# Kernel tuning notes

Measured on AMD Instinct MI355X. Metric: run time of the kernel, lower is better.

Reference implementation:

```python
import jax, jax.numpy as jnp
import numpy as np

B, S, D, H, HS = 4, 2048, 1024, 16, 64
DFF = 4 * D
EPS = 1e-5


def setup_inputs() -> dict:
    key = jax.random.key(0)
    ks = jax.random.split(key, 16)
    std = 0.02
    return {
        "x": jax.random.normal(ks[0], (B, S, D), jnp.float32),
        "Wq": jax.random.normal(ks[1], (H, D, HS), jnp.float32) * std,
        "bq": jnp.zeros((H, HS), jnp.float32),
        "Wk": jax.random.normal(ks[2], (H, D, HS), jnp.float32) * std,
        "bk": jnp.zeros((H, HS), jnp.float32),
        "Wv": jax.random.normal(ks[3], (H, D, HS), jnp.float32) * std,
        "bv": jnp.zeros((H, HS), jnp.float32),
        "Wp": jax.random.normal(ks[4], (D, D), jnp.float32) * std,
        "bp": jnp.zeros((D,), jnp.float32),
        "ln1_w": jnp.ones((D,), jnp.float32),
        "ln1_b": jnp.zeros((D,), jnp.float32),
        "ln2_w": jnp.ones((D,), jnp.float32),
        "ln2_b": jnp.zeros((D,), jnp.float32),
        "W1": jax.random.normal(ks[5], (D, DFF), jnp.float32) * std,
        "b1": jnp.zeros((DFF,), jnp.float32),
        "W2": jax.random.normal(ks[6], (DFF, D), jnp.float32) * std,
        "b2": jnp.zeros((D,), jnp.float32),
    }


def _layernorm(x, w, b):
    mu = jnp.mean(x, axis=-1, keepdims=True)
    var = jnp.mean(jnp.square(x - mu), axis=-1, keepdims=True)
    return (x - mu) * jax.lax.rsqrt(var + EPS) * w + b


def _block(x, Wq, bq, Wk, bk, Wv, bv, Wp, bp, ln1_w, ln1_b, ln2_w, ln2_b, W1, b1, W2, b2):
    seq = x.shape[1]
    xn = _layernorm(x, ln1_w, ln1_b)
    # batched per-head projections: [B,H,S,HS]
    q = jnp.einsum('bsd,hdk->bhsk', xn, Wq) + bq[:, None, :]
    k = jnp.einsum('bsd,hdk->bhsk', xn, Wk) + bk[:, None, :]
    v = jnp.einsum('bsd,hdk->bhsk', xn, Wv) + bv[:, None, :]
    scores = jnp.einsum('bhsk,bhtk->bhst', q, k)
    mask = jnp.tril(jnp.ones((seq, seq), bool))
    # original: masked_fill(-inf) then divide by sqrt(head_size) -> equivalent
    scores = jnp.where(mask, scores / jnp.sqrt(jnp.float32(HS)), -jnp.inf)
    attn = jax.nn.softmax(scores, axis=-1)
    out = jnp.einsum('bhst,bhtk->bhsk', attn, v)
    out = out.transpose(0, 2, 1, 3).reshape(x.shape[0], seq, H * HS)
    att = out @ Wp + bp
    x = x + att
    xn2 = _layernorm(x, ln2_w, ln2_b)
    h = jax.nn.gelu(xn2 @ W1 + b1, approximate=False)  # torch nn.GELU default = exact
    ffn = h @ W2 + b2
    return x + ffn


def reference(x, Wq, bq, Wk, bk, Wv, bv, Wp, bp, ln1_w, ln1_b, ln2_w, ln2_b, W1, b1, W2, b2):
    out = _block(x, Wq, bq, Wk, bk, Wv, bv, Wp, bp, ln1_w, ln1_b, ln2_w, ln2_b, W1, b1, W2, b2)
    return out
```

## Files before the change

kernel.cpp:

```cpp
#include <hip/hip_runtime.h>
#include <hip/hip_bf16.h>

#define D_MODEL 1024
#define SEQ 2048
#define NH 16
#define HSZ 64
#define DFF_ 4096

typedef __attribute__((ext_vector_type(8))) short short8;
typedef __attribute__((ext_vector_type(4))) short short4v;
typedef __attribute__((ext_vector_type(4))) float f32x4;

static __device__ __forceinline__ short f2bf(float f) {
  unsigned u = __builtin_bit_cast(unsigned, f);
  u = u + 0x7fffu + ((u >> 16) & 1u);
  return (short)(u >> 16);
}

static __device__ __forceinline__ unsigned packbf2(float a, float b) {
  return (unsigned)(unsigned short)f2bf(a) | ((unsigned)(unsigned short)f2bf(b) << 16);
}

static __device__ __forceinline__ f32x4 mfma16(short8 a, short8 b, f32x4 c) {
  return __builtin_amdgcn_mfma_f32_16x16x32_bf16(a, b, c, 0, 0, 0);
}

static __device__ __forceinline__ void gld16(const short* g, short* l) {
  __builtin_amdgcn_global_load_lds((const __attribute__((address_space(1))) void*)g,
                                   (__attribute__((address_space(3))) void*)l, 16, 0, 0);
}

__global__ void transpose_qkv_kernel(const float* __restrict__ Wq, const float* __restrict__ Wk,
                                     const float* __restrict__ Wv, short* __restrict__ dst) {
  __shared__ float tile[32][33];
  const int z = blockIdx.z;
  const int which = z >> 4, hh = z & 15;
  const float* src = (which == 0 ? Wq : which == 1 ? Wk : Wv) + (long)hh * (D_MODEL * HSZ);
  const int c0 = blockIdx.x * 32, r0 = blockIdx.y * 32;
  const int tx = threadIdx.x, ty = threadIdx.y;
#pragma unroll
  for (int i = 0; i < 4; ++i)
    tile[ty + 8 * i][tx] = src[(long)(r0 + ty + 8 * i) * HSZ + c0 + tx];
  __syncthreads();
#pragma unroll
  for (int i = 0; i < 4; ++i)
    dst[((long)which * 1024 + hh * 64 + c0 + ty + 8 * i) * D_MODEL + r0 + tx] =
        f2bf(tile[tx][ty + 8 * i]);
}

__global__ void transpose_gen_kernel(const float* __restrict__ src, short* __restrict__ dst,
                                     int R, int C) {
  __shared__ float tile[32][33];
  const int c0 = blockIdx.x * 32, r0 = blockIdx.y * 32;
  const int tx = threadIdx.x, ty = threadIdx.y;
#pragma unroll
  for (int i = 0; i < 4; ++i)
    tile[ty + 8 * i][tx] = src[(long)(r0 + ty + 8 * i) * C + c0 + tx];
  __syncthreads();
#pragma unroll
  for (int i = 0; i < 4; ++i)
    dst[(long)(c0 + ty + 8 * i) * R + r0 + tx] = f2bf(tile[tx][ty + 8 * i]);
}

__global__ void v_transpose_kernel(const short* __restrict__ vb, short* __restrict__ vt) {
  __shared__ short tile[64 * 72];
  const int bh = blockIdx.y;
  const int t0 = blockIdx.x * 64;
  const long base = (long)bh * SEQ * HSZ;
  const int tid = threadIdx.x;
  const int r = tid >> 3, c = (tid & 7) * 8;
#pragma unroll
  for (int it = 0; it < 2; ++it) {
    const int rr = r + it * 32;
    *(short8*)&tile[rr * 72 + c] = *(const short8*)(vb + base + (long)(t0 + rr) * HSZ + c);
  }
  __syncthreads();
#pragma unroll
  for (int it = 0; it < 2; ++it) {
    const int rr = r + it * 32;
    short8 o;
#pragma unroll
    for (int u = 0; u < 8; ++u) o[u] = tile[(c + u) * 72 + rr];
    *(short8*)(vt + base + (long)rr * SEQ + t0 + c) = o;
  }
}

__global__ void ln_kernel(const float* __restrict__ x, const float* __restrict__ w,
                          const float* __restrict__ b, short* __restrict__ out) {
  const int row = blockIdx.x;
  const float* xr = x + (size_t)row * D_MODEL;
  const int t = threadIdx.x;
  float4 v = *(const float4*)(xr + t * 4);
  float s = v.x + v.y + v.z + v.w;
  float s2 = v.x * v.x + v.y * v.y + v.z * v.z + v.w * v.w;
#pragma unroll
  for (int o = 1; o < 64; o <<= 1) {
    s += __shfl_xor(s, o, 64);
    s2 += __shfl_xor(s2, o, 64);
  }
  __shared__ float ps[8];
  const int lane = t & 63, wid = t >> 6;
  if (lane == 0) { ps[wid] = s; ps[wid + 4] = s2; }
  __syncthreads();
  s = ps[0] + ps[1] + ps[2] + ps[3];
  s2 = ps[4] + ps[5] + ps[6] + ps[7];
  const float mu = s * (1.0f / D_MODEL);
  const float var = s2 * (1.0f / D_MODEL) - mu * mu;
  const float rs = rsqrtf(var + 1e-5f);
  float4 wv = *(const float4*)(w + t * 4);
  float4 bv = *(const float4*)(b + t * 4);
  short4v o4;
  o4[0] = f2bf((v.x - mu) * rs * wv.x + bv.x);
  o4[1] = f2bf((v.y - mu) * rs * wv.y + bv.y);
  o4[2] = f2bf((v.z - mu) * rs * wv.z + bv.z);
  o4[3] = f2bf((v.w - mu) * rs * wv.w + bv.w);
  *(short4v*)(out + (size_t)row * D_MODEL + t * 4) = o4;
}

#define BM 128
#define BN 128

template <int MODE>
__global__ void gemm_kernel(const short* __restrict__ A, const short* __restrict__ Bt,
                            const int K, const float* __restrict__ c0,
                            const float* __restrict__ c1, const float* __restrict__ c2,
                            const float* __restrict__ res, void* __restrict__ o0,
                            void* __restrict__ o1, void* __restrict__ o2) {
  __shared__ short As[2 * BM * 32];
  __shared__ short Bs[2 * BM * 32];
  const int tid = threadIdx.x;
  const int lane = tid & 63, wid = tid >> 6;
  const int wm = wid >> 1, wn = wid & 1;
  const int l16 = lane & 15, lg = lane >> 4;
  const long r0 = (long)blockIdx.y * BM;
  const long n0 = (long)blockIdx.x * BN;

  f32x4 acc[4][4];
#pragma unroll
  for (int m = 0; m < 4; ++m)
#pragma unroll
    for (int n = 0; n < 4; ++n) {
      f32x4 z = {0.f, 0.f, 0.f, 0.f};
      acc[m][n] = z;
    }

  const int sr = lane >> 2;
  const int sc = (lane & 3) * 8;
  const short* ga0 = A + (r0 + wid * 16 + sr) * (long)K + sc;
  const short* ga1 = ga0 + 64 * (long)K;
  const short* gb0 = Bt + (n0 + wid * 16 + sr) * (long)K + sc;
  const short* gb1 = gb0 + 64 * (long)K;
  short* la0 = &As[wid * 16 * 32];
  short* la1 = la0 + 64 * 32;
  short* lb0 = &Bs[wid * 16 * 32];
  short* lb1 = lb0 + 64 * 32;

  for (int kt = 0; kt < K; kt += 64) {
    __syncthreads();
#pragma unroll
    for (int p = 0; p < 2; ++p) {
      gld16(ga0 + kt + p * 32, la0 + p * (BM * 32));
      gld16(ga1 + kt + p * 32, la1 + p * (BM * 32));
      gld16(gb0 + kt + p * 32, lb0 + p * (BM * 32));
      gld16(gb1 + kt + p * 32, lb1 + p * (BM * 32));
    }
    __syncthreads();
#pragma unroll
    for (int p = 0; p < 2; ++p) {
      short8 af[4], bfr[4];
#pragma unroll
      for (int m = 0; m < 4; ++m)
        af[m] = *(const short8*)&As[p * (BM * 32) + (wm * 64 + m * 16 + l16) * 32 + lg * 8];
#pragma unroll
      for (int n = 0; n < 4; ++n)
        bfr[n] = *(const short8*)&Bs[p * (BM * 32) + (wn * 64 + n * 16 + l16) * 32 + lg * 8];
#pragma unroll
      for (int m = 0; m < 4; ++m)
#pragma unroll
        for (int n = 0; n < 4; ++n) acc[m][n] = mfma16(af[m], bfr[n], acc[m][n]);
    }
  }

#pragma unroll
  for (int m = 0; m < 4; ++m) {
    const long rowb = r0 + wm * 64 + m * 16 + lg * 4;
#pragma unroll
    for (int n = 0; n < 4; ++n) {
      const long col = n0 + wn * 64 + n * 16 + l16;
#pragma unroll
      for (int j = 0; j < 4; ++j) {
        float val = acc[m][n][j];
        const long rr = rowb + j;
        if (MODE == 0) {
          const int c10 = (int)col & 1023;
          const int which = (int)col >> 10;
          const float* bb = which == 0 ? c0 : which == 1 ? c1 : c2;
          short* oo = (short*)(which == 0 ? o0 : which == 1 ? o1 : o2);
          val += bb[c10];
          const long bidx = rr >> 11, sidx = rr & 2047;
          const int h = c10 >> 6, hs = c10 & 63;
          oo[(((bidx * NH) + h) * SEQ + sidx) * HSZ + hs] = f2bf(val);
        } else if (MODE == 1) {
          val += c0[col] + res[rr * D_MODEL + col];
          ((float*)o0)[rr * D_MODEL + col] = val;
        } else if (MODE == 2) {
          val += c0[col];
          const float g = 0.5f * val * (1.0f + erff(val * 0.70710678118654752f));
          ((short*)o0)[rr * DFF_ + col] = f2bf(g);
        } else {
          val += c0[col] + res[rr * D_MODEL + col];
          ((float*)o0)[rr * D_MODEL + col] = val;
        }
      }
    }
  }
}

#define SM_SCALE 0.18033688011112042f

__global__ void attn_kernel(const short* __restrict__ q, const short* __restrict__ k,
                            const short* __restrict__ vt, short* __restrict__ att) {
  const int qt = (SEQ / 128 - 1) - (int)blockIdx.y;
  const int bh = blockIdx.x;
  const int b = bh >> 4, h = bh & 15;
  const int tid = threadIdx.x;
  const int lane = tid & 63, wq = tid >> 6;
  const int l16 = lane & 15, lg = lane >> 4;
  const long base = (long)bh * SEQ * HSZ;

  __shared__ short Ks[64 * 72];
  __shared__ short Vts[64 * 72];
  __shared__ short Ps[4 * 32 * 72];
  short* Psw = &Ps[wq * 32 * 72];

  const int R0 = qt * 128 + wq * 32;

  short8 qf[2][2];
#pragma unroll
  for (int qn = 0; qn < 2; ++qn)
#pragma unroll
    for (int kk = 0; kk < 2; ++kk)
      qf[qn][kk] =
          *(const short8*)(q + base + (long)(R0 + qn * 16 + l16) * HSZ + kk * 32 + lg * 8);

  float m_[2] = {-INFINITY, -INFINITY};
  float l_[2] = {0.f, 0.f};
  f32x4 oacc[2][4];
#pragma unroll
  for (int qn = 0; qn < 2; ++qn)
#pragma unroll
    for (int hf = 0; hf < 4; ++hf) {
      f32x4 z = {0.f, 0.f, 0.f, 0.f};
      oacc[qn][hf] = z;
    }

  const int srow = tid >> 3, scol = (tid & 7) * 8;
  const int tend = (qt + 1) * 128;

  for (int t0 = 0; t0 < tend; t0 += 64) {
    __syncthreads();
#pragma unroll
    for (int it = 0; it < 2; ++it) {
      const int r = srow + it * 32;
      *(short8*)&Ks[r * 72 + scol] =
          *(const short8*)(k + base + (long)(t0 + r) * HSZ + scol);
      *(short8*)&Vts[r * 72 + scol] =
          *(const short8*)(vt + base + (long)r * SEQ + t0 + scol);
    }
    __syncthreads();

    if (t0 <= R0 + 31) {
      f32x4 sf[4][2];
#pragma unroll
      for (int tt = 0; tt < 4; ++tt)
#pragma unroll
        for (int qn = 0; qn < 2; ++qn) {
          f32x4 z = {0.f, 0.f, 0.f, 0.f};
          sf[tt][qn] = z;
        }
      __builtin_amdgcn_s_setprio(1);
#pragma unroll
      for (int kk = 0; kk < 2; ++kk)
#pragma unroll
        for (int tt = 0; tt < 4; ++tt) {
          short8 kf = *(const short8*)&Ks[(tt * 16 + l16) * 72 + kk * 32 + lg * 8];
#pragma unroll
          for (int qn = 0; qn < 2; ++qn) sf[tt][qn] = mfma16(kf, qf[qn][kk], sf[tt][qn]);
        }
      __builtin_amdgcn_s_setprio(0);

      const bool domask = (t0 + 63 > R0);
      const int tb = t0 + lg * 4;
#pragma unroll
      for (int tt = 0; tt < 4; ++tt)
#pragma unroll
        for (int qn = 0; qn < 2; ++qn) {
          const int qg = R0 + qn * 16 + l16;
#pragma unroll
          for (int j = 0; j < 4; ++j) {
            float s = sf[tt][qn][j] * SM_SCALE;
            if (domask && (tb + tt * 16 + j > qg)) s = -INFINITY;
            sf[tt][qn][j] = s;
          }
        }

      float mx[2];
#pragma unroll
      for (int qn = 0; qn < 2; ++qn) {
        float m0 = sf[0][qn][0];
#pragma unroll
        for (int tt = 0; tt < 4; ++tt)
#pragma unroll
          for (int j = 0; j < 4; ++j) m0 = fmaxf(m0, sf[tt][qn][j]);
        m0 = fmaxf(m0, __shfl_xor(m0, 16, 64));
        m0 = fmaxf(m0, __shfl_xor(m0, 32, 64));
        mx[qn] = m0;
      }
      const int ok = (mx[0] <= m_[0] + 8.f) && (mx[1] <= m_[1] + 8.f);
      if (!__all(ok)) {
#pragma unroll
        for (int qn = 0; qn < 2; ++qn) {
          const float mnew = fmaxf(m_[qn], mx[qn]);
          const float rc = exp2f(m_[qn] - mnew);
          m_[qn] = mnew;
          l_[qn] *= rc;
#pragma unroll
          for (int hf = 0; hf < 4; ++hf)
#pragma unroll
            for (int j = 0; j < 4; ++j) oacc[qn][hf][j] *= rc;
        }
      }
#pragma unroll
      for (int qn = 0; qn < 2; ++qn) {
        float sum = 0.f;
#pragma unroll
        for (int tt = 0; tt < 4; ++tt)
#pragma unroll
          for (int j = 0; j < 4; ++j) {
            const float p = exp2f(sf[tt][qn][j] - m_[qn]);
            sf[tt][qn][j] = p;
            sum += p;
          }
        l_[qn] += sum;
      }

#pragma unroll
      for (int qn = 0; qn < 2; ++qn)
#pragma unroll
        for (int tt = 0; tt < 4; ++tt) {
          const int ro = (qn * 16 + l16) * 72 + tt * 16 + lg * 4;
          *(unsigned*)&Psw[ro] = packbf2(sf[tt][qn][0], sf[tt][qn][1]);
          *(unsigned*)&Psw[ro + 2] = packbf2(sf[tt][qn][2], sf[tt][qn][3]);
        }

      __builtin_amdgcn_s_setprio(1);
#pragma unroll
      for (int kk = 0; kk < 2; ++kk) {
        short8 pa[2];
#pragma unroll
        for (int qn = 0; qn < 2; ++qn)
          pa[qn] = *(const short8*)&Psw[(qn * 16 + l16) * 72 + kk * 32 + lg * 8];
#pragma unroll
        for (int hf = 0; hf < 4; ++hf) {
          short8 vf = *(const short8*)&Vts[(hf * 16 + l16) * 72 + kk * 32 + lg * 8];
#pragma unroll
          for (int qn = 0; qn < 2; ++qn)
            oacc[qn][hf] = mfma16(vf, pa[qn], oacc[qn][hf]);
        }
      }
      __builtin_amdgcn_s_setprio(0);
    }
  }

#pragma unroll
  for (int qn = 0; qn < 2; ++qn) {
    float lt = l_[qn];
    lt += __shfl_xor(lt, 16, 64);
    lt += __shfl_xor(lt, 32, 64);
    const float inv = 1.0f / lt;
    const long row = R0 + qn * 16 + l16;
#pragma unroll
    for (int hf = 0; hf < 4; ++hf) {
      short4v o4;
#pragma unroll
      for (int j = 0; j < 4; ++j) o4[j] = f2bf(oacc[qn][hf][j] * inv);
      *(short4v*)(att + ((long)b * SEQ + row) * D_MODEL + h * HSZ + hf * 16 + lg * 4) = o4;
    }
  }
}

extern "C" void kernel_launch(void* const* d_in, const int* in_sizes, int n_in,
                              void* d_out, int out_size, void* d_ws, size_t ws_size,
                              hipStream_t stream) {
  const float* x = (const float*)d_in[0];
  const float* Wq = (const float*)d_in[1];
  const float* bq = (const float*)d_in[2];
  const float* Wk = (const float*)d_in[3];
  const float* bk = (const float*)d_in[4];
  const float* Wv = (const float*)d_in[5];
  const float* bv = (const float*)d_in[6];
  const float* Wp = (const float*)d_in[7];
  const float* bp = (const float*)d_in[8];
  const float* g1 = (const float*)d_in[9];
  const float* be1 = (const float*)d_in[10];
  const float* g2 = (const float*)d_in[11];
  const float* be2 = (const float*)d_in[12];
  const float* W1 = (const float*)d_in[13];
  const float* b1 = (const float*)d_in[14];
  const float* W2 = (const float*)d_in[15];
  const float* b2 = (const float*)d_in[16];
  float* out = (float*)d_out;
  char* ws = (char*)d_ws;

  if (ws_size < 209715200ull) return;

  short* WqkvT = (short*)(ws + 0);
  short* WpT = (short*)(ws + 6291456);
  short* W1T = (short*)(ws + 8388608);
  short* W2T = (short*)(ws + 16777216);
  short* xn = (short*)(ws + 25165824);
  short* vt = (short*)(ws + 25165824);
  short* qb = (short*)(ws + 41943040);
  short* kb = (short*)(ws + 58720256);
  short* vb = (short*)(ws + 75497472);
  short* att = (short*)(ws + 92274688);
  float* x1 = (float*)(ws + 109051904);
  short* hb = (short*)(ws + 142606336);

  dim3 tb(32, 8);
  transpose_qkv_kernel<<<dim3(2, 32, 48), tb, 0, stream>>>(Wq, Wk, Wv, WqkvT);
  transpose_gen_kernel<<<dim3(32, 32), tb, 0, stream>>>(Wp, WpT, 1024, 1024);
  transpose_gen_kernel<<<dim3(128, 32), tb, 0, stream>>>(W1, W1T, 1024, 4096);
  transpose_gen_kernel<<<dim3(32, 128), tb, 0, stream>>>(W2, W2T, 4096, 1024);
  ln_kernel<<<8192, 256, 0, stream>>>(x, g1, be1, xn);
  gemm_kernel<0><<<dim3(24, 64), 256, 0, stream>>>(xn, WqkvT, 1024, bq, bk, bv, nullptr,
                                                   qb, kb, vb);
  v_transpose_kernel<<<dim3(32, 64), 256, 0, stream>>>(vb, vt);
  attn_kernel<<<dim3(64, 16), 256, 0, stream>>>(qb, kb, vt, att);
  gemm_kernel<1><<<dim3(8, 64), 256, 0, stream>>>(att, WpT, 1024, bp, nullptr, nullptr, x,
                                                  x1, nullptr, nullptr);
  ln_kernel<<<8192, 256, 0, stream>>>(x1, g2, be2, xn);
  gemm_kernel<2><<<dim3(32, 64), 256, 0, stream>>>(xn, W1T, 1024, b1, nullptr, nullptr,
                                                   nullptr, hb, nullptr, nullptr);
  gemm_kernel<3><<<dim3(8, 64), 256, 0, stream>>>(hb, W2T, 4096, b2, nullptr, nullptr, x1,
                                                  out, nullptr, nullptr);
}
```

Before: 463.0 us.

## Enlarge GEMM tiles with double-buffered prefetch and XOR-swizzled LDS layouts

The GEMM kernel moves to 512-thread blocks with 256-column tiles and 128 or 256 rows selected by a template parameter. It double-buffers LDS and issues the next K-tile's global-to-LDS loads spread across the MFMA loop, using one barrier per iteration instead of two. LDS rows are XOR-swizzled instead of padded to avoid bank conflicts, and the attention K/V tiles get the same swizzle. The aim is more data reuse per block and load latency hidden behind MFMA work, at the cost of more LDS and registers per block and fewer blocks for the N=1024 GEMMs.

```diff
diff --git a/kernel.cpp b/kernel.cpp
--- a/kernel.cpp
+++ b/kernel.cpp
@@ -117,73 +117,100 @@
   *(short4v*)(out + (size_t)row * D_MODEL + t * 4) = o4;
 }
 
-#define BM 128
-#define BN 128
-
-template <int MODE>
-__global__ void gemm_kernel(const short* __restrict__ A, const short* __restrict__ Bt,
-                            const int K, const float* __restrict__ c0,
-                            const float* __restrict__ c1, const float* __restrict__ c2,
-                            const float* __restrict__ res, void* __restrict__ o0,
-                            void* __restrict__ o1, void* __restrict__ o2) {
-  __shared__ short As[2 * BM * 32];
-  __shared__ short Bs[2 * BM * 32];
+template <int MODE, int TM>
+__global__ __launch_bounds__(512, 2) void gemm_kernel(
+    const short* __restrict__ A, const short* __restrict__ Bt, const int K,
+    const float* __restrict__ c0, const float* __restrict__ c1,
+    const float* __restrict__ c2, const float* __restrict__ res,
+    void* __restrict__ o0, void* __restrict__ o1, void* __restrict__ o2) {
+  constexpr int MF = TM / 32;
+  constexpr int NA = TM / 64;
+  constexpr int NS = NA + 4;
+  __shared__ short As[2][TM * 64];
+  __shared__ short Bs[2][256 * 64];
   const int tid = threadIdx.x;
   const int lane = tid & 63, wid = tid >> 6;
-  const int wm = wid >> 1, wn = wid & 1;
+  const int wm = wid >> 2, wn = wid & 3;
   const int l16 = lane & 15, lg = lane >> 4;
-  const long r0 = (long)blockIdx.y * BM;
-  const long n0 = (long)blockIdx.x * BN;
-
-  f32x4 acc[4][4];
-#pragma unroll
-  for (int m = 0; m < 4; ++m)
+  const long r0 = (long)blockIdx.y * TM;
+  const long n0 = (long)blockIdx.x * 256;
+
+  long offA[NA], offB[4];
+#pragma unroll
+  for (int i = 0; i < NA; ++i) {
+    const int o = wid * 64 + lane + i * 512;
+    const int row = o >> 3, slot = o & 7;
+    offA[i] = (long)(r0 + row) * K + ((slot ^ (row & 7)) << 3);
+  }
+#pragma unroll
+  for (int i = 0; i < 4; ++i) {
+    const int o = wid * 64 + lane + i * 512;
+    const int row = o >> 3, slot = o & 7;
+    offB[i] = (long)(n0 + row) * K + ((slot ^ (row & 7)) << 3);
+  }
+
+  f32x4 acc[MF][4];
+#pragma unroll
+  for (int m = 0; m < MF; ++m)
 #pragma unroll
     for (int n = 0; n < 4; ++n) {
       f32x4 z = {0.f, 0.f, 0.f, 0.f};
       acc[m][n] = z;
     }
 
-  const int sr = lane >> 2;
-  const int sc = (lane & 3) * 8;
-  const short* ga0 = A + (r0 + wid * 16 + sr) * (long)K + sc;
-  const short* ga1 = ga0 + 64 * (long)K;
-  const short* gb0 = Bt + (n0 + wid * 16 + sr) * (long)K + sc;
-  const short* gb1 = gb0 + 64 * (long)K;
-  short* la0 = &As[wid * 16 * 32];
-  short* la1 = la0 + 64 * 32;
-  short* lb0 = &Bs[wid * 16 * 32];
-  short* lb1 = lb0 + 64 * 32;
-
-  for (int kt = 0; kt < K; kt += 64) {
+  const int x7 = l16 & 7;
+  const int psl0 = (lg ^ x7) * 8, psl1 = ((4 + lg) ^ x7) * 8;
+  const int aBase = (wm * (TM / 2) + l16) * 64;
+  const int bBase = (wn * 64 + l16) * 64;
+
+  const int NT = K >> 6;
+#pragma unroll
+  for (int i = 0; i < NA; ++i) gld16(A + offA[i], &As[0][(wid * 64 + i * 512) * 8]);
+#pragma unroll
+  for (int i = 0; i < 4; ++i) gld16(Bt + offB[i], &Bs[0][(wid * 64 + i * 512) * 8]);
+  __syncthreads();
+
+  for (int t = 0; t < NT; ++t) {
+    const int cur = t & 1;
+    const int kt = t << 6;
+    const short* Ac = As[cur];
+    const short* Bc = Bs[cur];
+    const bool hasnext = (t + 1 < NT);
+    short8 bfr[4][2];
+#pragma unroll
+    for (int n = 0; n < 4; ++n) {
+      bfr[n][0] = *(const short8*)&Bc[bBase + n * 1024 + psl0];
+      bfr[n][1] = *(const short8*)&Bc[bBase + n * 1024 + psl1];
+    }
+#pragma unroll
+    for (int m = 0; m < MF; ++m) {
+      if (hasnext) {
+        const int s0 = (m * NS) / MF, s1 = ((m + 1) * NS) / MF;
+#pragma unroll
+        for (int s = s0; s < s1; ++s) {
+          if (s < NA)
+            gld16(A + offA[s] + kt + 64, &As[cur ^ 1][(wid * 64 + s * 512) * 8]);
+          else
+            gld16(Bt + offB[s - NA] + kt + 64,
+                  &Bs[cur ^ 1][(wid * 64 + (s - NA) * 512) * 8]);
+        }
+      }
+      const short8 a0 = *(const short8*)&Ac[aBase + m * 1024 + psl0];
+      const short8 a1 = *(const short8*)&Ac[aBase + m * 1024 + psl1];
+      __builtin_amdgcn_s_setprio(1);
+#pragma unroll
+      for (int n = 0; n < 4; ++n) {
+        acc[m][n] = mfma16(a0, bfr[n][0], acc[m][n]);
+        acc[m][n] = mfma16(a1, bfr[n][1], acc[m][n]);
+      }
+      __builtin_amdgcn_s_setprio(0);
+    }
     __syncthreads();
-#pragma unroll
-    for (int p = 0; p < 2; ++p) {
-      gld16(ga0 + kt + p * 32, la0 + p * (BM * 32));
-      gld16(ga1 + kt + p * 32, la1 + p * (BM * 32));
-      gld16(gb0 + kt + p * 32, lb0 + p * (BM * 32));
-      gld16(gb1 + kt + p * 32, lb1 + p * (BM * 32));
-    }
-    __syncthreads();
-#pragma unroll
-    for (int p = 0; p < 2; ++p) {
-      short8 af[4], bfr[4];
-#pragma unroll
-      for (int m = 0; m < 4; ++m)
-        af[m] = *(const short8*)&As[p * (BM * 32) + (wm * 64 + m * 16 + l16) * 32 + lg * 8];
-#pragma unroll
-      for (int n = 0; n < 4; ++n)
-        bfr[n] = *(const short8*)&Bs[p * (BM * 32) + (wn * 64 + n * 16 + l16) * 32 + lg * 8];
-#pragma unroll
-      for (int m = 0; m < 4; ++m)
-#pragma unroll
-        for (int n = 0; n < 4; ++n) acc[m][n] = mfma16(af[m], bfr[n], acc[m][n]);
-    }
-  }
-
-#pragma unroll
-  for (int m = 0; m < 4; ++m) {
-    const long rowb = r0 + wm * 64 + m * 16 + lg * 4;
+  }
+
+#pragma unroll
+  for (int m = 0; m < MF; ++m) {
+    const long rowb = r0 + wm * (TM / 2) + m * 16 + lg * 4;
 #pragma unroll
     for (int n = 0; n < 4; ++n) {
       const long col = n0 + wn * 64 + n * 16 + l16;
@@ -228,8 +255,8 @@
   const int l16 = lane & 15, lg = lane >> 4;
   const long base = (long)bh * SEQ * HSZ;
 
-  __shared__ short Ks[64 * 72];
-  __shared__ short Vts[64 * 72];
+  __shared__ short Ks[64 * 64];
+  __shared__ short Vts[64 * 64];
   __shared__ short Ps[4 * 32 * 72];
   short* Psw = &Ps[wq * 32 * 72];
 
@@ -254,7 +281,10 @@
       oacc[qn][hf] = z;
     }
 
-  const int srow = tid >> 3, scol = (tid & 7) * 8;
+  const int srow = tid >> 3, wg = tid & 7;
+  const int swc = (wg ^ (srow & 7)) * 8;
+  const int x7 = l16 & 7;
+  const int rc0 = (lg ^ x7) * 8, rc1 = ((4 + lg) ^ x7) * 8;
   const int tend = (qt + 1) * 128;
 
   for (int t0 = 0; t0 < tend; t0 += 64) {
@@ -262,10 +292,10 @@
 #pragma unroll
     for (int it = 0; it < 2; ++it) {
       const int r = srow + it * 32;
-      *(short8*)&Ks[r * 72 + scol] =
-          *(const short8*)(k + base + (long)(t0 + r) * HSZ + scol);
-      *(short8*)&Vts[r * 72 + scol] =
-          *(const short8*)(vt + base + (long)r * SEQ + t0 + scol);
+      const short8 kv = *(const short8*)(k + base + (long)(t0 + r) * HSZ + wg * 8);
+      const short8 vv = *(const short8*)(vt + base + (long)r * SEQ + t0 + wg * 8);
+      *(short8*)&Ks[r * 64 + swc] = kv;
+      *(short8*)&Vts[r * 64 + swc] = vv;
     }
     __syncthreads();
 
@@ -283,7 +313,7 @@
       for (int kk = 0; kk < 2; ++kk)
 #pragma unroll
         for (int tt = 0; tt < 4; ++tt) {
-          short8 kf = *(const short8*)&Ks[(tt * 16 + l16) * 72 + kk * 32 + lg * 8];
+          short8 kf = *(const short8*)&Ks[(tt * 16 + l16) * 64 + (kk ? rc1 : rc0)];
 #pragma unroll
           for (int qn = 0; qn < 2; ++qn) sf[tt][qn] = mfma16(kf, qf[qn][kk], sf[tt][qn]);
         }
@@ -362,7 +392,7 @@
           pa[qn] = *(const short8*)&Psw[(qn * 16 + l16) * 72 + kk * 32 + lg * 8];
 #pragma unroll
         for (int hf = 0; hf < 4; ++hf) {
-          short8 vf = *(const short8*)&Vts[(hf * 16 + l16) * 72 + kk * 32 + lg * 8];
+          short8 vf = *(const short8*)&Vts[(hf * 16 + l16) * 64 + (kk ? rc1 : rc0)];
 #pragma unroll
           for (int qn = 0; qn < 2; ++qn)
             oacc[qn][hf] = mfma16(vf, pa[qn], oacc[qn][hf]);
@@ -433,15 +463,16 @@
   transpose_gen_kernel<<<dim3(128, 32), tb, 0, stream>>>(W1, W1T, 1024, 4096);
   transpose_gen_kernel<<<dim3(32, 128), tb, 0, stream>>>(W2, W2T, 4096, 1024);
   ln_kernel<<<8192, 256, 0, stream>>>(x, g1, be1, xn);
-  gemm_kernel<0><<<dim3(24, 64), 256, 0, stream>>>(xn, WqkvT, 1024, bq, bk, bv, nullptr,
-                                                   qb, kb, vb);
+  gemm_kernel<0, 256><<<dim3(12, 32), 512, 0, stream>>>(xn, WqkvT, 1024, bq, bk, bv,
+                                                        nullptr, qb, kb, vb);
   v_transpose_kernel<<<dim3(32, 64), 256, 0, stream>>>(vb, vt);
   attn_kernel<<<dim3(64, 16), 256, 0, stream>>>(qb, kb, vt, att);
-  gemm_kernel<1><<<dim3(8, 64), 256, 0, stream>>>(att, WpT, 1024, bp, nullptr, nullptr, x,
-                                                  x1, nullptr, nullptr);
+  gemm_kernel<1, 128><<<dim3(4, 64), 512, 0, stream>>>(att, WpT, 1024, bp, nullptr,
+                                                       nullptr, x, x1, nullptr, nullptr);
   ln_kernel<<<8192, 256, 0, stream>>>(x1, g2, be2, xn);
-  gemm_kernel<2><<<dim3(32, 64), 256, 0, stream>>>(xn, W1T, 1024, b1, nullptr, nullptr,
-                                                   nullptr, hb, nullptr, nullptr);
-  gemm_kernel<3><<<dim3(8, 64), 256, 0, stream>>>(hb, W2T, 4096, b2, nullptr, nullptr, x1,
-                                                  out, nullptr, nullptr);
-}
+  gemm_kernel<2, 256><<<dim3(16, 32), 512, 0, stream>>>(xn, W1T, 1024, b1, nullptr,
+                                                        nullptr, nullptr, hb, nullptr,
+                                                        nullptr);
+  gemm_kernel<3, 128><<<dim3(4, 64), 512, 0, stream>>>(hb, W2T, 4096, b2, nullptr,
+                                                       nullptr, x1, out, nullptr, nullptr);
+}
```

Result: slower. 486.9 us (+5.2%).
